# Performance work log

Hardware: AMD Instinct MI355X
Metric: run time of the kernel (lower is better)

## Reference

```python
import jax, jax.numpy as jnp
import numpy as np
import math

EPS = 1e-6


def _pixel_index(loc_orig, H, W):
    # loc_orig in [-1,1] -> nearest pixel index on HxW grid (matches torch round/clamp)
    loc = jnp.clip(loc_orig, -1.0, 1.0)
    loc = (loc + 1.0) * 0.5
    px = jnp.clip(jnp.round(loc[..., 0] * (W - 1)).astype(jnp.int32), 0, W - 1)
    py = jnp.clip(jnp.round(loc[..., 1] * (H - 1)).astype(jnp.int32), 0, H - 1)
    return py * W + px  # [B, N0]


def token2map(x, loc_orig, idx_agg, H, W):
    # scatter token features to an HxW map, averaging over points landing in a pixel
    B, N, C = x.shape
    N0 = idx_agg.shape[1]
    pix = _pixel_index(loc_orig, H, W)
    pix_f = (pix + jnp.arange(B)[:, None] * (H * W)).reshape(-1)  # [B*N0]
    cnt = jax.ops.segment_sum(jnp.ones((B * N0,), x.dtype), pix_f, num_segments=B * H * W) + EPS
    val = 1.0 / cnt[pix_f]
    tok_feat = x[jnp.arange(B)[:, None], idx_agg].reshape(B * N0, C)  # gather token feat per point
    x_map = jax.ops.segment_sum(tok_feat * val[:, None], pix_f, num_segments=B * H * W)
    return x_map.reshape(B, H, W, C).transpose(0, 3, 1, 2)  # NCHW


def map2token(x_map, N, loc_orig, idx_agg, agg_weight):
    # gather nearest-pixel map features back to tokens, agg_weight-normalized per token
    B, C, H, W = x_map.shape
    N0 = idx_agg.shape[1]
    pix = _pixel_index(loc_orig, H, W)
    pix_f = (pix + jnp.arange(B)[:, None] * (H * W)).reshape(-1)
    tok_f = (idx_agg + jnp.arange(B)[:, None] * N).reshape(-1)
    w = agg_weight.reshape(B * N0)
    wsum = jax.ops.segment_sum(w, tok_f, num_segments=B * N) + EPS
    val = w / wsum[tok_f]
    pix_feat = x_map.transpose(0, 2, 3, 1).reshape(B * H * W, C)[pix_f]
    return jax.ops.segment_sum(pix_feat * val[:, None], tok_f, num_segments=B * N).reshape(B, N, C)


def farthest_point_sample(x, npoint):
    # deterministic FPS (seed index 0), sequential by nature -> fori_loop
    x = jax.lax.stop_gradient(x)
    B, N, C = x.shape
    def body(i, state):
        dist, far, cent = state
        cent = cent.at[:, i].set(far)
        c = x[jnp.arange(B), far]  # [B,C]
        d = jnp.sum((x - c[:, None, :]) ** 2, axis=-1)
        dist = jnp.minimum(dist, d)
        far = jnp.argmax(dist, axis=-1).astype(jnp.int32)
        return dist, far, cent
    init = (jnp.full((B, N), 1e10, x.dtype), jnp.zeros((B,), jnp.int32), jnp.zeros((B, npoint), jnp.int32))
    _, _, cent = jax.lax.fori_loop(0, npoint, body, init)
    return cent


def merge_tokens_agg_dist2(x, index_down, x_down, idx_agg):
    # assign each token to nearest sampled center (argmin of distance), average-merge
    B, N, C = x.shape
    Ns = x_down.shape[1]
    d2 = (jnp.sum(x * x, -1)[:, :, None] + jnp.sum(x_down * x_down, -1)[:, None, :]
          - 2.0 * jnp.einsum('bnc,bsc->bns', x, x_down))  # squared dist; same argmin as cdist
    idx_t = jnp.argmin(d2, axis=2).astype(jnp.int32)  # [B,N]
    # sampled centers merge to themselves
    idx_t = idx_t.at[jnp.arange(B)[:, None], index_down].set(jnp.arange(Ns, dtype=jnp.int32)[None, :])
    idx_f = (idx_t + jnp.arange(B)[:, None] * Ns).reshape(-1)
    allw = jax.ops.segment_sum(jnp.ones((B * N,), x.dtype), idx_f, num_segments=B * Ns) + EPS
    norm_w = (1.0 / allw[idx_f]).reshape(B, N)  # weight=None -> ones
    x_merged = jax.ops.segment_sum(x.reshape(B * N, C) * norm_w.reshape(-1, 1), idx_f,
                                   num_segments=B * Ns).reshape(B, Ns, C)
    idx_agg_new = jnp.take_along_axis(idx_t, idx_agg, axis=1)  # [B,N0]
    weight_t = jnp.take_along_axis(norm_w, idx_agg, axis=1)[..., None]  # [B,N0,1]
    return x_merged, idx_agg_new, weight_t


def down_layer_forward(x, loc_orig, idx_agg, agg_weight, conv_w, conv_b, skip_w, H, W, sample_ratio=0.25):
    B, N, Cin = x.shape
    # TokenConv: token2map -> 3x3 stride-2 conv -> map2token + 1x1 skip
    x_map = token2map(x, loc_orig, idx_agg, H, W)
    x_map = jax.lax.conv_general_dilated(x_map, conv_w, window_strides=(2, 2),
                                         padding=((1, 1), (1, 1)),
                                         dimension_numbers=('NCHW', 'OIHW', 'NCHW'))
    x_map = x_map + conv_b[None, :, None, None]
    x_tok = map2token(x_map, N, loc_orig, idx_agg, agg_weight[..., 0])
    x = x_tok + jnp.einsum('bnc,oc->bno', x, skip_w)
    Ns = max(math.ceil(N * sample_ratio), 1)
    index_down = farthest_point_sample(x, Ns)
    x_down = x[jnp.arange(B)[:, None], index_down]  # index_points
    x_down, idx_agg_down, weight_t = merge_tokens_agg_dist2(x, index_down, x_down, idx_agg)
    agg_weight_down = agg_weight * weight_t
    agg_weight_down = agg_weight_down / jnp.max(agg_weight_down, axis=1, keepdims=True)
    return x_down, idx_agg_down, agg_weight_down


def setup_inputs() -> dict:
    key = jax.random.key(0)
    ks = jax.random.split(key, 6)
    B, N, N0, Cin, Cout, H, W = 8, 3136, 12544, 64, 128, 112, 112
    x = jax.random.normal(ks[0], (B, N, Cin), jnp.float32)
    loc_orig = jax.random.uniform(ks[1], (B, N0, 2), jnp.float32, -1.0, 1.0)
    idx_agg = jax.random.randint(ks[2], (B, N0), 0, N)
    agg_weight = jax.random.uniform(ks[3], (B, N0, 1), jnp.float32, 0.1, 1.0)
    conv_w = jax.random.normal(ks[4], (Cout, Cin, 3, 3), jnp.float32) * (1.0 / np.sqrt(Cin * 9))
    conv_b = jnp.zeros((Cout,), jnp.float32)
    skip_w = jax.random.normal(ks[5], (Cout, Cin), jnp.float32) * (1.0 / np.sqrt(Cin))
    return {"x": x, "loc_orig": loc_orig, "idx_agg": idx_agg, "agg_weight": agg_weight,
            "conv_w": conv_w, "conv_b": conv_b, "skip_w": skip_w, "H": H, "W": W}


def reference(x, loc_orig, idx_agg, agg_weight, conv_w, conv_b, skip_w, H, W):
    return down_layer_forward(x, loc_orig, idx_agg, agg_weight, conv_w, conv_b, skip_w, H, W)
```

## Files before the change

### kernel.cpp

```cpp
#include <hip/hip_runtime.h>
#include <cstdint>

#define EPSF 1e-6f

constexpr int B = 8, N = 3136, N0 = 12544, CIN = 64, COUT = 128;
constexpr int H = 112, W = 112, HW = H * W;
constexpr int HO = 56, WO = 56, OHW = HO * WO;
constexpr int NS = 784;

constexpr size_t o_xmap = 0;
constexpr size_t sz_xmap = (size_t)B * HW * CIN * 4;
constexpr size_t o_cnt  = o_xmap + sz_xmap;
constexpr size_t sz_cnt = (size_t)B * HW * 4;
constexpr size_t o_wsum = o_cnt + sz_cnt;
constexpr size_t sz_wsum = (size_t)B * N * 4;
constexpr size_t o_maxw = o_wsum + sz_wsum;
constexpr size_t sz_maxw = 32;
constexpr size_t o_zpad = o_maxw + sz_maxw;
constexpr size_t sz_zpad = 256;
constexpr size_t zero_end = o_zpad + sz_zpad;
constexpr size_t o_wt   = (zero_end + 255) & ~(size_t)255;
constexpr size_t o_swt  = o_wt + 576 * 128 * 4;
constexpr size_t o_pixf = o_swt + 64 * 128 * 4;
constexpr size_t o_conv = o_pixf + (size_t)B * N0 * 4;
constexpr size_t o_xnew = o_conv + (size_t)B * OHW * 128 * 4;
constexpr size_t o_sqn  = o_xnew + (size_t)B * N * 128 * 4;
constexpr size_t o_normw = o_sqn + (size_t)B * N * 4;
constexpr size_t o_idxt = o_normw + (size_t)B * N * 4;
constexpr size_t o_d2   = (o_idxt + (size_t)B * N * 4 + 255) & ~(size_t)255;
constexpr size_t D2B = (size_t)N * N * 4;

__device__ inline unsigned tkey(float v) {
    unsigned u = __float_as_uint(v);
    unsigned m = (unsigned)((int)u >> 31);
    return u ^ (m | 0x80000000u);
}

__global__ void k_transpose(const float* __restrict__ conv_w, const float* __restrict__ skip_w,
                            float* __restrict__ wT, float* __restrict__ swt) {
    int g = blockIdx.x * 256 + threadIdx.x;
    if (g < 576 * 128) {
        int k = g >> 7, co = g & 127;
        int kpos = k >> 6, ci = k & 63;
        wT[g] = conv_w[(co * 64 + ci) * 9 + kpos];
    } else {
        int g2 = g - 576 * 128;
        if (g2 < 64 * 128) {
            int ci = g2 >> 7, co = g2 & 127;
            swt[g2] = skip_w[co * 64 + ci];
        }
    }
}

__global__ void k_pix_cnt(const float* __restrict__ loc, int* __restrict__ pixf,
                          float* __restrict__ cnt) {
    int g = blockIdx.x * 256 + threadIdx.x;
    if (g >= B * N0) return;
    int b = g / N0;
    float lx = loc[2 * g], ly = loc[2 * g + 1];
    lx = fminf(fmaxf(lx, -1.f), 1.f);
    ly = fminf(fmaxf(ly, -1.f), 1.f);
    int px = (int)rintf((lx + 1.f) * 0.5f * 111.f); px = min(max(px, 0), 111);
    int py = (int)rintf((ly + 1.f) * 0.5f * 111.f); py = min(max(py, 0), 111);
    int pf = b * HW + py * W + px;
    pixf[g] = pf;
    atomicAdd(&cnt[pf], 1.f);
}

__global__ void k_token2map(const float* __restrict__ x, const int* __restrict__ idx_agg,
                            const int* __restrict__ pixf, const float* __restrict__ cnt,
                            float* __restrict__ xmap) {
    int t = blockIdx.x * 256 + threadIdx.x;
    int g = t >> 6, c = t & 63;
    if (g >= B * N0) return;
    int pf = pixf[g];
    float val = 1.f / (cnt[pf] + EPSF);
    int b = g / N0;
    int tok = idx_agg[g];
    float xv = x[((size_t)(b * N + tok)) * 64 + c];
    atomicAdd(&xmap[(size_t)pf * 64 + c], xv * val);
}

__global__ __launch_bounds__(128) void k_conv(const float* __restrict__ xmap,
                                              const float* __restrict__ wT,
                                              const float* __restrict__ cb,
                                              const float* __restrict__ zpad,
                                              float* __restrict__ conv_out) {
    int co = threadIdx.x;
    int wo0 = blockIdx.x * 8, ho = blockIdx.y, b = blockIdx.z;
    float acc[8];
    float bias = cb[co];
#pragma unroll
    for (int p = 0; p < 8; p++) acc[p] = bias;
    for (int kh = 0; kh < 3; ++kh) {
        int iy = 2 * ho + kh - 1;
        bool vy = (iy >= 0 && iy < H);
        for (int kw = 0; kw < 3; ++kw) {
            const float* wp = wT + (size_t)((kh * 3 + kw) * 64) * 128 + co;
            const float* bp[8];
#pragma unroll
            for (int p = 0; p < 8; p++) {
                int ix = 2 * (wo0 + p) + kw - 1;
                bool v = vy && ix >= 0 && ix < W;
                bp[p] = v ? (xmap + ((size_t)b * HW + iy * W + ix) * 64) : zpad;
            }
#pragma unroll 4
            for (int ci = 0; ci < 64; ++ci) {
                float wv = wp[(size_t)ci * 128];
#pragma unroll
                for (int p = 0; p < 8; p++) acc[p] = fmaf(bp[p][ci], wv, acc[p]);
            }
        }
    }
    size_t ob = ((size_t)b * OHW + ho * WO + wo0) * 128 + co;
#pragma unroll
    for (int p = 0; p < 8; p++) conv_out[ob + (size_t)p * 128] = acc[p];
}

__global__ void k_wsum(const int* __restrict__ idx_agg, const float* __restrict__ aggw,
                       float* __restrict__ wsum) {
    int g = blockIdx.x * 256 + threadIdx.x;
    if (g >= B * N0) return;
    int b = g / N0;
    atomicAdd(&wsum[(size_t)b * N + idx_agg[g]], aggw[g]);
}

__global__ void k_skip(const float* __restrict__ x, const float* __restrict__ swt,
                       float* __restrict__ xnew) {
    int t = blockIdx.x * 256 + threadIdx.x;
    int g = t >> 7, co = t & 127;
    const float* xr = x + (size_t)g * 64;
    float acc = 0.f;
#pragma unroll 8
    for (int ci = 0; ci < 64; ++ci) acc = fmaf(xr[ci], swt[ci * 128 + co], acc);
    xnew[t] = acc;
}

__global__ void k_map2token(const float* __restrict__ loc, const int* __restrict__ idx_agg,
                            const float* __restrict__ aggw, const float* __restrict__ wsum,
                            const float* __restrict__ conv_out, float* __restrict__ xnew) {
    int t = blockIdx.x * 256 + threadIdx.x;
    int g = t >> 7, co = t & 127;
    if (g >= B * N0) return;
    int b = g / N0;
    float lx = loc[2 * g], ly = loc[2 * g + 1];
    lx = fminf(fmaxf(lx, -1.f), 1.f);
    ly = fminf(fmaxf(ly, -1.f), 1.f);
    int px = (int)rintf((lx + 1.f) * 0.5f * 55.f); px = min(max(px, 0), 55);
    int py = (int)rintf((ly + 1.f) * 0.5f * 55.f); py = min(max(py, 0), 55);
    int opix = py * WO + px;
    int tok = idx_agg[g];
    float val = aggw[g] / (wsum[(size_t)b * N + tok] + EPSF);
    float feat = conv_out[((size_t)b * OHW + opix) * 128 + co];
    atomicAdd(&xnew[((size_t)b * N + tok) * 128 + co], feat * val);
}

__global__ void k_sqn(const float* __restrict__ xnew, float* __restrict__ sqn) {
    int tid = threadIdx.x;
    int wid = tid >> 6, lane = tid & 63;
    int row = blockIdx.x * 4 + wid;
    const float* xr = xnew + (size_t)row * 128;
    float2 v = *(const float2*)(xr + lane * 2);
    float s = v.x * v.x + v.y * v.y;
#pragma unroll
    for (int off = 32; off > 0; off >>= 1) s += __shfl_xor(s, off, 64);
    if (lane == 0) sqn[row] = s;
}

__global__ __launch_bounds__(256) void k_d2gemm(const float* __restrict__ xnew,
                                                const float* __restrict__ sqn,
                                                unsigned* __restrict__ d2, int b_off) {
    __shared__ float As[64 * 132];
    __shared__ float Bs[64 * 132];
    int tid = threadIdx.x;
    int tx = tid & 15, ty = tid >> 4;
    int bx = blockIdx.x, by = blockIdx.y, cb = blockIdx.z;
    int b = b_off + cb;
    int ri0 = by * 64, rj0 = bx * 64;
    const float* xb = xnew + (size_t)b * N * 128;
#pragma unroll
    for (int q = 0; q < 8; q++) {
        int f4 = tid + q * 256;
        int r = f4 >> 5, k4 = (f4 & 31) << 2;
        *(float4*)&As[r * 132 + k4] = *(const float4*)(xb + (size_t)(ri0 + r) * 128 + k4);
        *(float4*)&Bs[r * 132 + k4] = *(const float4*)(xb + (size_t)(rj0 + r) * 128 + k4);
    }
    __syncthreads();
    float acc[4][4] = {};
    const float* Ap = As + (ty * 4) * 132;
    const float* Bp = Bs + (tx * 4) * 132;
    for (int kk = 0; kk < 32; ++kk) {
        int k = kk * 4;
        float4 a[4], bb[4];
#pragma unroll
        for (int u = 0; u < 4; u++) a[u] = *(const float4*)(Ap + u * 132 + k);
#pragma unroll
        for (int v = 0; v < 4; v++) bb[v] = *(const float4*)(Bp + v * 132 + k);
#pragma unroll
        for (int u = 0; u < 4; u++)
#pragma unroll
            for (int v = 0; v < 4; v++) {
                acc[u][v] = fmaf(a[u].x, bb[v].x, acc[u][v]);
                acc[u][v] = fmaf(a[u].y, bb[v].y, acc[u][v]);
                acc[u][v] = fmaf(a[u].z, bb[v].z, acc[u][v]);
                acc[u][v] = fmaf(a[u].w, bb[v].w, acc[u][v]);
            }
    }
    const float* sq = sqn + (size_t)b * N;
    float4 sb = *(const float4*)(sq + rj0 + tx * 4);
    unsigned* d2c = d2 + (size_t)cb * N * N;
#pragma unroll
    for (int u = 0; u < 4; u++) {
        int rowg = ri0 + ty * 4 + u;
        float sqa = sq[rowg];
        uint4 o;
        o.x = tkey(sqa + sb.x - 2.f * acc[u][0]);
        o.y = tkey(sqa + sb.y - 2.f * acc[u][1]);
        o.z = tkey(sqa + sb.z - 2.f * acc[u][2]);
        o.w = tkey(sqa + sb.w - 2.f * acc[u][3]);
        *(uint4*)(d2c + (size_t)rowg * N + rj0 + tx * 4) = o;
    }
}

template <int CTRL, int RMASK>
__device__ __forceinline__ unsigned long long dppmax64(unsigned long long k) {
    unsigned lo = (unsigned)k, hi = (unsigned)(k >> 32);
    unsigned slo = (unsigned)__builtin_amdgcn_update_dpp((int)lo, (int)lo, CTRL, RMASK, 0xF, false);
    unsigned shi = (unsigned)__builtin_amdgcn_update_dpp((int)hi, (int)hi, CTRL, RMASK, 0xF, false);
    unsigned long long o = ((unsigned long long)shi << 32) | slo;
    return o > k ? o : k;
}
__device__ __forceinline__ unsigned long long rdlane64(unsigned long long k, int l) {
    unsigned lo = (unsigned)__builtin_amdgcn_readlane((int)(unsigned)k, l);
    unsigned hi = (unsigned)__builtin_amdgcn_readlane((int)(k >> 32), l);
    return ((unsigned long long)hi << 32) | lo;
}

__global__ __launch_bounds__(256) void k_fps6(const unsigned* __restrict__ d2,
                                              int* __restrict__ idx_t,
                                              float* __restrict__ normw, int b_off) {
    int tid = threadIdx.x;
    int lane = tid & 63, wid = tid >> 6;
    int b = b_off + blockIdx.x;
    const unsigned* D2b = d2 + (size_t)blockIdx.x * (size_t)N * N;
    __shared__ unsigned long long slot[2][4];
    __shared__ int cent_l[NS];
    __shared__ int it_l[N];
    __shared__ float cntw[NS];
    const bool full = (tid < 16);
    const unsigned KI = tkey(1e10f);
    unsigned kd[16];
    int am[16];
#pragma unroll
    for (int r = 0; r < 4; r++)
#pragma unroll
        for (int c = 0; c < 4; c++) { kd[r * 4 + c] = (r < 3 || full) ? KI : 0u; am[r * 4 + c] = 0; }

    int far = 0;
    for (int s = 0; s < NS; ++s) {
        if (tid == 0) cent_l[s] = far;
        const unsigned* row = D2b + (size_t)far * N;
        uint4 v0 = *(const uint4*)(row + tid * 4);
        uint4 v1 = *(const uint4*)(row + 1024 + tid * 4);
        uint4 v2 = *(const uint4*)(row + 2048 + tid * 4);
        uint4 v3 = full ? *(const uint4*)(row + 3072 + tid * 4) : make_uint4(0, 0, 0, 0);
        uint4 vv[4] = {v0, v1, v2, v3};
#pragma unroll
        for (int r = 0; r < 4; r++) {
            unsigned e[4] = {vv[r].x, vv[r].y, vv[r].z, vv[r].w};
#pragma unroll
            for (int c = 0; c < 4; c++)
                if (e[c] < kd[r * 4 + c]) { kd[r * 4 + c] = e[c]; am[r * 4 + c] = s; }
        }
        if (s == NS - 1) break;
        unsigned tmax = kd[0];
#pragma unroll
        for (int q = 1; q < 16; q++) tmax = max(tmax, kd[q]);
        unsigned il = 4095u;
#pragma unroll
        for (int r = 3; r >= 0; --r)
#pragma unroll
            for (int c = 3; c >= 0; --c)
                if (kd[r * 4 + c] == tmax) il = (unsigned)(r * 1024 + tid * 4 + c);
        unsigned long long key = ((unsigned long long)tmax << 12) | (unsigned long long)(4095u - il);
        key = dppmax64<0xB1, 0xF>(key);
        key = dppmax64<0x4E, 0xF>(key);
        key = dppmax64<0x141, 0xF>(key);
        key = dppmax64<0x140, 0xF>(key);
        key = dppmax64<0x142, 0xA>(key);
        key = dppmax64<0x143, 0xC>(key);
        unsigned long long wmax = rdlane64(key, 63);
        int cur = s & 1;
        if (lane == 0) slot[cur][wid] = wmax;
        asm volatile("s_waitcnt lgkmcnt(0)\n\ts_barrier" ::: "memory");
        unsigned long long s0 = slot[cur][0], s1 = slot[cur][1];
        unsigned long long s2 = slot[cur][2], s3 = slot[cur][3];
        unsigned long long m0 = s0 > s1 ? s0 : s1;
        unsigned long long m1 = s2 > s3 ? s2 : s3;
        unsigned long long win = m0 > m1 ? m0 : m1;
        far = 4095 - (int)(win & 0xFFFull);
    }
    __syncthreads();
#pragma unroll
    for (int r = 0; r < 4; r++) {
        if (r == 3 && !full) break;
        int i0 = r * 1024 + tid * 4;
        *(int4*)&it_l[i0] = make_int4(am[r * 4 + 0], am[r * 4 + 1], am[r * 4 + 2], am[r * 4 + 3]);
    }
    for (int t = tid; t < NS; t += 256) cntw[t] = 0.f;
    __syncthreads();
    for (int t = tid; t < NS; t += 256) it_l[cent_l[t]] = t;
    __syncthreads();
    for (int i = tid; i < N; i += 256) atomicAdd(&cntw[it_l[i]], 1.f);
    __syncthreads();
    int* it = idx_t + (size_t)b * N;
    float* nw = normw + (size_t)b * N;
    for (int i = tid; i < N; i += 256) {
        int t = it_l[i];
        it[i] = t;
        nw[i] = 1.f / (cntw[t] + EPSF);
    }
}

__device__ inline unsigned long long packkey(float v, unsigned i) {
    unsigned u = __float_as_uint(v);
    u = (u & 0x80000000u) ? ~u : (u | 0x80000000u);
    return ((unsigned long long)u << 32) | (unsigned long long)(0xFFFFFFFFu - i);
}

__global__ __launch_bounds__(1024) void k_fps0(const float* __restrict__ xnew,
                                               const float* __restrict__ sqn,
                                               int* __restrict__ idx_t,
                                               float* __restrict__ normw, int b_off) {
    int tid = threadIdx.x;
    int b = b_off + blockIdx.x;
    __shared__ unsigned long long slot[2];
    __shared__ int cent[NS];
    __shared__ float cntw[NS];
    __shared__ float csh[128];
    if (tid == 0) { slot[0] = 0ull; slot[1] = 0ull; }
    if (tid < NS) cntw[tid] = 0.f;
    float dist[4] = {1e10f, 1e10f, 1e10f, 1e10f};
    int amin[4] = {0, 0, 0, 0};
    float sqi[4];
#pragma unroll
    for (int r = 0; r < 4; r++) {
        int i = tid + r * 1024;
        if (i < N) sqi[r] = sqn[(size_t)b * N + i];
    }
    __syncthreads();
    int far = 0;
    for (int s = 0; s < NS; ++s) {
        int cur = s & 1;
        if (tid == 0) { cent[s] = far; slot[cur ^ 1] = 0ull; }
        if (tid < 128) csh[tid] = xnew[((size_t)b * N + far) * 128 + tid];
        float sqf = sqn[(size_t)b * N + far];
        __syncthreads();
        unsigned long long key = 0ull;
#pragma unroll
        for (int r = 0; r < 4; r++) {
            int i = tid + r * 1024;
            if (i < N) {
                const float* xr = xnew + ((size_t)b * N + i) * 128;
                float dot = 0.f;
#pragma unroll 8
                for (int k = 0; k < 128; k++) dot = fmaf(xr[k], csh[k], dot);
                float d = sqi[r] + sqf - 2.f * dot;
                if (d < dist[r]) { dist[r] = d; amin[r] = s; }
                unsigned long long k2 = packkey(dist[r], (unsigned)i);
                if (k2 > key) key = k2;
            }
        }
#pragma unroll
        for (int off = 32; off > 0; off >>= 1) {
            unsigned long long o = __shfl_xor(key, off, 64);
            if (o > key) key = o;
        }
        if ((tid & 63) == 0) atomicMax(&slot[cur], key);
        __syncthreads();
        unsigned long long kk = slot[cur];
        far = (int)(0xFFFFFFFFu - (unsigned)(kk & 0xFFFFFFFFull));
        __syncthreads();
    }
    int* it = idx_t + (size_t)b * N;
#pragma unroll
    for (int r = 0; r < 4; r++) { int i = tid + r * 1024; if (i < N) it[i] = amin[r]; }
    __syncthreads();
    if (tid < NS) it[cent[tid]] = tid;
    __syncthreads();
#pragma unroll
    for (int r = 0; r < 4; r++) { int i = tid + r * 1024; if (i < N) atomicAdd(&cntw[it[i]], 1.f); }
    __syncthreads();
    float* nw = normw + (size_t)b * N;
#pragma unroll
    for (int r = 0; r < 4; r++) {
        int i = tid + r * 1024;
        if (i < N) nw[i] = 1.f / (cntw[it[i]] + EPSF);
    }
}

__global__ void k_merge_scatter(const float* __restrict__ xnew, const int* __restrict__ idx_t,
                                const float* __restrict__ normw, float* __restrict__ out0) {
    int t = blockIdx.x * 256 + threadIdx.x;
    int g = t >> 7, co = t & 127;
    if (g >= B * N) return;
    int b = g / N;
    int s = idx_t[g];
    float nwv = normw[g];
    atomicAdd(&out0[((size_t)b * NS + s) * 128 + co], xnew[(size_t)g * 128 + co] * nwv);
}

__global__ void k_out12(const int* __restrict__ idx_agg, const float* __restrict__ aggw,
                        const int* __restrict__ idx_t, const float* __restrict__ normw,
                        float* __restrict__ out1, float* __restrict__ out2,
                        unsigned* __restrict__ maxw) {
    int tid = threadIdx.x;
    int q = blockIdx.x * 256 + tid;
    int b = q / N0;
    int tok = idx_agg[q];
    int it = idx_t[(size_t)b * N + tok];
    out1[q] = (float)it;
    float aw = aggw[q] * normw[(size_t)b * N + tok];
    out2[q] = aw;
    float m = aw;
#pragma unroll
    for (int off = 32; off > 0; off >>= 1) m = fmaxf(m, __shfl_xor(m, off, 64));
    __shared__ float wmax[4];
    int lane = tid & 63, wid = tid >> 6;
    if (lane == 0) wmax[wid] = m;
    __syncthreads();
    if (tid == 0) {
        float mm = fmaxf(fmaxf(wmax[0], wmax[1]), fmaxf(wmax[2], wmax[3]));
        atomicMax(&maxw[b], __float_as_uint(mm));
    }
}

__global__ void k_out2div(float* __restrict__ out2, const unsigned* __restrict__ maxw) {
    int q = blockIdx.x * 256 + threadIdx.x;
    if (q >= B * N0) return;
    int b = q / N0;
    out2[q] = out2[q] / __uint_as_float(maxw[b]);
}

extern "C" void kernel_launch(void* const* d_in, const int* in_sizes, int n_in,
                              void* d_out, int out_size, void* d_ws, size_t ws_size,
                              hipStream_t stream) {
    const float* x = (const float*)d_in[0];
    const float* loc = (const float*)d_in[1];
    const int* idx_agg = (const int*)d_in[2];
    const float* aggw = (const float*)d_in[3];
    const float* conv_w = (const float*)d_in[4];
    const float* conv_b = (const float*)d_in[5];
    const float* skip_w = (const float*)d_in[6];

    char* ws = (char*)d_ws;
    float* xmap = (float*)(ws + o_xmap);
    float* cnt = (float*)(ws + o_cnt);
    float* wsum = (float*)(ws + o_wsum);
    unsigned* maxw = (unsigned*)(ws + o_maxw);
    float* zpad = (float*)(ws + o_zpad);
    float* wT = (float*)(ws + o_wt);
    float* swt = (float*)(ws + o_swt);
    int* pixf = (int*)(ws + o_pixf);
    float* conv_out = (float*)(ws + o_conv);
    float* xnew = (float*)(ws + o_xnew);
    float* sqn = (float*)(ws + o_sqn);
    float* normw = (float*)(ws + o_normw);
    int* idx_t = (int*)(ws + o_idxt);
    unsigned* d2 = (unsigned*)(ws + o_d2);

    float* out0 = (float*)d_out;
    float* out1 = out0 + (size_t)B * NS * COUT;
    float* out2 = out1 + (size_t)B * N0;

    hipMemsetAsync(d_ws, 0, zero_end, stream);
    hipMemsetAsync(d_out, 0, (size_t)B * NS * COUT * 4, stream);

    k_transpose<<<(576 * 128 + 64 * 128 + 255) / 256, 256, 0, stream>>>(conv_w, skip_w, wT, swt);
    k_pix_cnt<<<(B * N0 + 255) / 256, 256, 0, stream>>>(loc, pixf, cnt);
    k_token2map<<<(B * N0 * 64) / 256, 256, 0, stream>>>(x, idx_agg, pixf, cnt, xmap);
    k_conv<<<dim3(7, 56, 8), 128, 0, stream>>>(xmap, wT, conv_b, zpad, conv_out);
    k_wsum<<<(B * N0 + 255) / 256, 256, 0, stream>>>(idx_agg, aggw, wsum);
    k_skip<<<(B * N * 128) / 256, 256, 0, stream>>>(x, swt, xnew);
    k_map2token<<<(B * N0 * 128) / 256, 256, 0, stream>>>(loc, idx_agg, aggw, wsum, conv_out, xnew);
    k_sqn<<<(B * N) / 4, 256, 0, stream>>>(xnew, sqn);

    size_t avail = ws_size > o_d2 ? ws_size - o_d2 : 0;
    int CB = (int)(avail / D2B);
    if (CB > B) CB = B;
    if (CB >= 1) {
        for (int b0 = 0; b0 < B; b0 += CB) {
            int nb = (B - b0 < CB) ? (B - b0) : CB;
            k_d2gemm<<<dim3(49, 49, nb), 256, 0, stream>>>(xnew, sqn, d2, b0);
            k_fps6<<<nb, 256, 0, stream>>>(d2, idx_t, normw, b0);
        }
    } else {
        k_fps0<<<B, 1024, 0, stream>>>(xnew, sqn, idx_t, normw, 0);
    }

    k_merge_scatter<<<(B * N * 128) / 256, 256, 0, stream>>>(xnew, idx_t, normw, out0);
    k_out12<<<(B * N0) / 256, 256, 0, stream>>>(idx_agg, aggw, idx_t, normw, out1, out2, maxw);
    k_out2div<<<(B * N0 + 255) / 256, 256, 0, stream>>>(out2, maxw);
}
```

Before: 2.180 ms.

## Exploit d2 symmetry in GEMM and speculatively prefetch runner-up FPS row

The pairwise distance GEMM now computes only upper-triangular tiles and writes each off-diagonal tile also in transposed form, roughly halving the arithmetic. The FPS kernel speculatively loads the row of the second-best candidate after each step and reuses it if that candidate becomes the next centroid, aiming to hide global load latency in the serial loop. The transposed stores are less coalesced, and the prefetch adds extra memory traffic when the guess misses.

Measured after the change: 2.244 ms. 2.9% more time.

```diff
diff --git a/kernel.cpp b/kernel.cpp
--- a/kernel.cpp
+++ b/kernel.cpp
@@ -170,11 +170,12 @@
 __global__ __launch_bounds__(256) void k_d2gemm(const float* __restrict__ xnew,
                                                 const float* __restrict__ sqn,
                                                 unsigned* __restrict__ d2, int b_off) {
+    int bx = blockIdx.x, by = blockIdx.y, cb = blockIdx.z;
+    if (by > bx) return;
     __shared__ float As[64 * 132];
     __shared__ float Bs[64 * 132];
     int tid = threadIdx.x;
     int tx = tid & 15, ty = tid >> 4;
-    int bx = blockIdx.x, by = blockIdx.y, cb = blockIdx.z;
     int b = b_off + cb;
     int ri0 = by * 64, rj0 = bx * 64;
     const float* xb = xnew + (size_t)b * N * 128;
@@ -209,6 +210,7 @@
     const float* sq = sqn + (size_t)b * N;
     float4 sb = *(const float4*)(sq + rj0 + tx * 4);
     unsigned* d2c = d2 + (size_t)cb * N * N;
+    unsigned okey[4][4];
 #pragma unroll
     for (int u = 0; u < 4; u++) {
         int rowg = ri0 + ty * 4 + u;
@@ -218,7 +220,16 @@
         o.y = tkey(sqa + sb.y - 2.f * acc[u][1]);
         o.z = tkey(sqa + sb.z - 2.f * acc[u][2]);
         o.w = tkey(sqa + sb.w - 2.f * acc[u][3]);
+        okey[u][0] = o.x; okey[u][1] = o.y; okey[u][2] = o.z; okey[u][3] = o.w;
         *(uint4*)(d2c + (size_t)rowg * N + rj0 + tx * 4) = o;
+    }
+    if (bx != by) {
+#pragma unroll
+        for (int v = 0; v < 4; v++) {
+            int colg = rj0 + tx * 4 + v;
+            uint4 m = make_uint4(okey[0][v], okey[1][v], okey[2][v], okey[3][v]);
+            *(uint4*)(d2c + (size_t)colg * N + ri0 + ty * 4) = m;
+        }
     }
 }
 
@@ -236,7 +247,7 @@
     return ((unsigned long long)hi << 32) | lo;
 }
 
-__global__ __launch_bounds__(256) void k_fps6(const unsigned* __restrict__ d2,
+__global__ __launch_bounds__(256) void k_fps7(const unsigned* __restrict__ d2,
                                               int* __restrict__ idx_t,
                                               float* __restrict__ normw, int b_off) {
     int tid = threadIdx.x;
@@ -256,14 +267,21 @@
 #pragma unroll
         for (int c = 0; c < 4; c++) { kd[r * 4 + c] = (r < 3 || full) ? KI : 0u; am[r * 4 + c] = 0; }
 
-    int far = 0;
+    int far = 0, far2 = -1;
+    uint4 p0 = make_uint4(0, 0, 0, 0), p1 = p0, p2 = p0, p3 = p0;
+
     for (int s = 0; s < NS; ++s) {
         if (tid == 0) cent_l[s] = far;
-        const unsigned* row = D2b + (size_t)far * N;
-        uint4 v0 = *(const uint4*)(row + tid * 4);
-        uint4 v1 = *(const uint4*)(row + 1024 + tid * 4);
-        uint4 v2 = *(const uint4*)(row + 2048 + tid * 4);
-        uint4 v3 = full ? *(const uint4*)(row + 3072 + tid * 4) : make_uint4(0, 0, 0, 0);
+        uint4 v0, v1, v2, v3;
+        if (far == far2) {
+            v0 = p0; v1 = p1; v2 = p2; v3 = p3;
+        } else {
+            const unsigned* row = D2b + (size_t)far * N;
+            v0 = *(const uint4*)(row + tid * 4);
+            v1 = *(const uint4*)(row + 1024 + tid * 4);
+            v2 = *(const uint4*)(row + 2048 + tid * 4);
+            v3 = full ? *(const uint4*)(row + 3072 + tid * 4) : make_uint4(0, 0, 0, 0);
+        }
         uint4 vv[4] = {v0, v1, v2, v3};
 #pragma unroll
         for (int r = 0; r < 4; r++) {
@@ -295,10 +313,18 @@
         asm volatile("s_waitcnt lgkmcnt(0)\n\ts_barrier" ::: "memory");
         unsigned long long s0 = slot[cur][0], s1 = slot[cur][1];
         unsigned long long s2 = slot[cur][2], s3 = slot[cur][3];
-        unsigned long long m0 = s0 > s1 ? s0 : s1;
-        unsigned long long m1 = s2 > s3 ? s2 : s3;
-        unsigned long long win = m0 > m1 ? m0 : m1;
+        unsigned long long m0 = s0 > s1 ? s0 : s1, q0 = s0 > s1 ? s1 : s0;
+        unsigned long long m1 = s2 > s3 ? s2 : s3, q1 = s2 > s3 ? s3 : s2;
+        unsigned long long win, run;
+        if (m0 >= m1) { win = m0; run = q0 > m1 ? q0 : m1; }
+        else          { win = m1; run = q1 > m0 ? q1 : m0; }
         far = 4095 - (int)(win & 0xFFFull);
+        far2 = 4095 - (int)(run & 0xFFFull);
+        const unsigned* prow = D2b + (size_t)far2 * N;
+        p0 = *(const uint4*)(prow + tid * 4);
+        p1 = *(const uint4*)(prow + 1024 + tid * 4);
+        p2 = *(const uint4*)(prow + 2048 + tid * 4);
+        p3 = full ? *(const uint4*)(prow + 3072 + tid * 4) : make_uint4(0, 0, 0, 0);
     }
     __syncthreads();
 #pragma unroll
@@ -492,7 +518,7 @@
         for (int b0 = 0; b0 < B; b0 += CB) {
             int nb = (B - b0 < CB) ? (B - b0) : CB;
             k_d2gemm<<<dim3(49, 49, nb), 256, 0, stream>>>(xnew, sqn, d2, b0);
-            k_fps6<<<nb, 256, 0, stream>>>(d2, idx_t, normw, b0);
+            k_fps7<<<nb, 256, 0, stream>>>(d2, idx_t, normw, b0);
         }
     } else {
         k_fps0<<<B, 1024, 0, stream>>>(xnew, sqn, idx_t, normw, 0);
```
